# Performance work log

Measured on AMD Instinct MI355X. Metric: run time of the kernel, lower is better.

## Reference

```python
import jax, jax.numpy as jnp
import numpy as np

N = 131072   # total nodes
G = 4096     # graphs
E = 524288   # directed bond edges
C = 96       # hidden_channels
L = 8        # num_layers
F_IN = 64    # atom features
NT = 5       # targets


def setup_inputs() -> dict:
    key = jax.random.key(0)
    ks = jax.random.split(key, 32)
    def rn(k, shape, s=0.05):
        return jax.random.normal(k, shape, jnp.float32) * s
    inp = {
        'x': jax.random.normal(ks[0], (N, F_IN), jnp.float32),
        'edge_index': jax.random.randint(ks[1], (2, E), 0, N),
        'batch': jnp.sort(jax.random.randint(ks[2], (N,), 0, G)),
        'num_graphs': G,
        # atom encoder
        'enc_w': rn(ks[3], (F_IN, C)), 'enc_b': rn(ks[4], (C,)),
        # virtual node embedding + MLP (Linear->BN->SiLU->Linear)
        'vn_emb': rn(ks[5], (C,)),
        'vn_w1': rn(ks[6], (C, C)), 'vn_b1': rn(ks[7], (C,)),
        'vn_g1': 1.0 + rn(ks[8], (C,)), 'vn_be1': rn(ks[9], (C,)),
        'vn_w2': rn(ks[10], (C, C)), 'vn_b2': rn(ks[11], (C,)),
        # per-layer GIN MLP (Linear C->2C, BN, SiLU, Linear 2C->C) stacked over L
        'conv_w1': rn(ks[12], (L, C, 2 * C)), 'conv_b1': rn(ks[13], (L, 2 * C)),
        'conv_g1': 1.0 + rn(ks[14], (L, 2 * C)), 'conv_be1': rn(ks[15], (L, 2 * C)),
        'conv_w2': rn(ks[16], (L, 2 * C, C)), 'conv_b2': rn(ks[17], (L, C)),
        # per-layer outer BatchNorm
        'bn_g': 1.0 + rn(ks[18], (L, C)), 'bn_b': rn(ks[19], (L, C)),
        # head: C->C/2 (BN,SiLU) -> C/4 (BN,SiLU) -> NT
        'h_w1': rn(ks[20], (C, C // 2)), 'h_b1': rn(ks[21], (C // 2,)),
        'h_g1': 1.0 + rn(ks[22], (C // 2,)), 'h_be1': rn(ks[23], (C // 2,)),
        'h_w2': rn(ks[24], (C // 2, C // 4)), 'h_b2': rn(ks[25], (C // 4,)),
        'h_g2': 1.0 + rn(ks[26], (C // 4,)), 'h_be2': rn(ks[27], (C // 4,)),
        'h_w3': rn(ks[28], (C // 4, NT)), 'h_b3': rn(ks[29], (NT,)),
    }
    return inp


def _bn(x, g, b, eps=1e-5):
    # training-mode BatchNorm1d: biased batch variance (matches torch normalization)
    m = x.mean(0)
    v = x.var(0)
    return (x - m) * jax.lax.rsqrt(v + eps) * g + b


def reference(x, edge_index, batch, num_graphs, enc_w, enc_b, vn_emb,
              vn_w1, vn_b1, vn_g1, vn_be1, vn_w2, vn_b2,
              conv_w1, conv_b1, conv_g1, conv_be1, conv_w2, conv_b2,
              bn_g, bn_b,
              h_w1, h_b1, h_g1, h_be1, h_w2, h_b2, h_g2, h_be2, h_w3, h_b3):
    n = x.shape[0]
    gN = int(num_graphs)
    c = enc_w.shape[1]
    nl = conv_w1.shape[0]

    h = x @ enc_w + enc_b                                   # [n, C]
    vn = jnp.broadcast_to(vn_emb, (gN, c))                  # virtual node feats
    h = jnp.concatenate([h, vn], 0)                         # [n+gN, C]

    # vectorized virtual-node edges: (n+batch[i]) <-> i, both directions
    node_ids = jnp.arange(n, dtype=batch.dtype)
    vidx = n + batch
    src = jnp.concatenate([edge_index[0], vidx, node_ids])
    tgt = jnp.concatenate([edge_index[1], node_ids, vidx])
    total = n + gN

    for i in range(nl):
        # GINConv, eps=0: MLP(x + sum_neighbors)
        agg = jax.ops.segment_sum(h[src], tgt, num_segments=total)
        z = h + agg
        z = z @ conv_w1[i] + conv_b1[i]
        z = jax.nn.silu(_bn(z, conv_g1[i], conv_be1[i]))
        z = z @ conv_w2[i] + conv_b2[i]
        z = jax.nn.silu(_bn(z, bn_g[i], bn_b[i]))           # outer BN + SiLU (dropout=eval)
        h = z if i == 0 else h + z                          # residual after layer 0
        if i < nl - 1:
            v = h[n:]
            v = jax.nn.silu(_bn(v @ vn_w1 + vn_b1, vn_g1, vn_be1)) @ vn_w2 + vn_b2
            h = jnp.concatenate([h[:n], v], 0)

    hn = h[:n]
    sums = jax.ops.segment_sum(hn, batch, num_segments=gN)
    counts = jax.ops.segment_sum(jnp.ones((n,), hn.dtype), batch, num_segments=gN)
    pooled = sums / jnp.maximum(counts, 1.0)[:, None]       # global_mean_pool

    z = jax.nn.silu(_bn(pooled @ h_w1 + h_b1, h_g1, h_be1))
    z = jax.nn.silu(_bn(z @ h_w2 + h_b2, h_g2, h_be2))
    return z @ h_w3 + h_b3                                  # [G, 5]
```

## Files before the change

### kernel.cpp

```cpp
#include <hip/hip_runtime.h>
#include <hip/hip_bf16.h>

constexpr int N_   = 131072;
constexpr int G_   = 4096;
constexpr int E_   = 524288;
constexpr int C_   = 96;
constexpr int L_   = 8;
constexpr int FIN_ = 64;
constexpr int TOT_ = N_ + G_;

typedef __attribute__((ext_vector_type(8))) short short8v;
typedef __attribute__((ext_vector_type(4))) float f32x4;
using bf16 = __hip_bfloat16;

__device__ __forceinline__ float silu_f(float y) { return y / (1.f + __expf(-y)); }
__device__ __forceinline__ float toF(float x) { return x; }
__device__ __forceinline__ float toF(bf16 x)  { return __bfloat162float(x); }
__device__ __forceinline__ float bfbits2f(short s) {
  return __uint_as_float(((unsigned)(unsigned short)s) << 16);
}
__device__ __forceinline__ short f2bfbits(float f) {
  bf16 b = __float2bfloat16(f);
  return *reinterpret_cast<short*>(&b);
}
__device__ __forceinline__ void atomAddD(double* p, double v) { unsafeAtomicAdd(p, v); }

static inline int gblk(long n) { return (int)((n + 255) / 256); }

__global__ __launch_bounds__(256) void k_prep(const float* __restrict__ enc_w,
    const float* __restrict__ conv_w1, const float* __restrict__ conv_w2,
    const float* __restrict__ vn_w1, const float* __restrict__ vn_w2,
    bf16* __restrict__ encwT, bf16* __restrict__ w1T, bf16* __restrict__ w2T,
    bf16* __restrict__ vnw1T, bf16* __restrict__ vnw2T) {
  int idx = blockIdx.x * 256 + threadIdx.x;
  const float* src; bf16* dst; int Kd, Nd, local;
  if (idx < 6144)        { src = enc_w;   dst = encwT; Kd = 64;  Nd = 96;  local = idx; }
  else if (idx < 153600) { src = conv_w1; dst = w1T;   Kd = 96;  Nd = 192; local = idx - 6144; }
  else if (idx < 301056) { src = conv_w2; dst = w2T;   Kd = 192; Nd = 96;  local = idx - 153600; }
  else if (idx < 310272) { src = vn_w1;   dst = vnw1T; Kd = 96;  Nd = 96;  local = idx - 301056; }
  else if (idx < 319488) { src = vn_w2;   dst = vnw2T; Kd = 96;  Nd = 96;  local = idx - 310272; }
  else return;
  int per = Kd * Nd;
  int i   = local / per;
  int rem = local - i * per;
  int k   = rem / Nd;
  int n   = rem - k * Nd;
  dst[(size_t)i * per + n * Kd + k] = __float2bfloat16(src[local]);
}

__global__ __launch_bounds__(256) void k_deg_count(const int* __restrict__ tgt, int* __restrict__ deg) {
  int e = blockIdx.x * 256 + threadIdx.x;
  if (e >= E_) return;
  atomicAdd(&deg[tgt[e]], 1);
}

__global__ __launch_bounds__(256) void k_scan_local(const int* __restrict__ deg, int* __restrict__ lp,
                                                    int* __restrict__ bsum) {
  __shared__ int s[256];
  int t = threadIdx.x;
  int i = blockIdx.x * 256 + t;
  int v = deg[i];
  s[t] = v;
  __syncthreads();
  for (int off = 1; off < 256; off <<= 1) {
    int x = (t >= off) ? s[t - off] : 0;
    __syncthreads();
    s[t] += x;
    __syncthreads();
  }
  lp[i] = s[t] - v;
  if (t == 255) bsum[blockIdx.x] = s[255];
}

__global__ __launch_bounds__(512) void k_scan_bsum(const int* __restrict__ bsum, int* __restrict__ boff) {
  __shared__ int s[512];
  int t = threadIdx.x;
  int v = bsum[t];
  s[t] = v;
  __syncthreads();
  for (int off = 1; off < 512; off <<= 1) {
    int x = (t >= off) ? s[t - off] : 0;
    __syncthreads();
    s[t] += x;
    __syncthreads();
  }
  boff[t] = s[t] - v;
}

__global__ __launch_bounds__(256) void k_scan_add(int* __restrict__ rs, const int* __restrict__ boff) {
  int i = blockIdx.x * 256 + threadIdx.x;
  if (i > N_) return;
  if (i == N_) { rs[N_] = E_; return; }
  rs[i] += boff[i >> 8];
}

__global__ __launch_bounds__(256) void k_csr_fill(const int* __restrict__ src, const int* __restrict__ tgt,
                                                  const int* __restrict__ rs, int* __restrict__ cur,
                                                  int* __restrict__ ssrc) {
  int e = blockIdx.x * 256 + threadIdx.x;
  if (e >= E_) return;
  int t = tgt[e];
  int pos = atomicAdd(&cur[t], 1);
  ssrc[rs[t] + pos] = src[e];
}

__global__ __launch_bounds__(256) void k_gbounds(const int* __restrict__ batch, int* __restrict__ gstart) {
  int i = blockIdx.x * 256 + threadIdx.x;
  if (i > N_) return;
  if (i == N_) {
    int last = batch[N_ - 1];
    for (int g = last + 1; g <= G_; ++g) gstart[g] = N_;
    return;
  }
  int b  = batch[i];
  int bp = (i == 0) ? -1 : batch[i - 1];
  for (int g = bp + 1; g <= b; ++g) gstart[g] = i;
}

__global__ __launch_bounds__(256) void k_deghist(const int* __restrict__ deg, int* __restrict__ hist) {
  __shared__ int lh[33];
  if (threadIdx.x < 33) lh[threadIdx.x] = 0;
  __syncthreads();
  int i = blockIdx.x * 256 + threadIdx.x;
  if (i < N_) {
    int b = deg[i]; if (b > 32) b = 32;
    atomicAdd(&lh[b], 1);
  }
  __syncthreads();
  if (threadIdx.x < 33 && lh[threadIdx.x] != 0) atomicAdd(&hist[threadIdx.x], lh[threadIdx.x]);
}

__global__ __launch_bounds__(64) void k_degbase(const int* __restrict__ hist, int* __restrict__ base) {
  if (threadIdx.x == 0) {
    int acc = 0;
    for (int b = 0; b < 33; ++b) { base[b] = acc; acc += hist[b]; }
  }
}

__global__ __launch_bounds__(256) void k_permfill(const int* __restrict__ deg, const int* __restrict__ base,
                                                  int* __restrict__ curs, int* __restrict__ perm) {
  __shared__ int lh[33];
  __shared__ int lbase[33];
  if (threadIdx.x < 33) lh[threadIdx.x] = 0;
  __syncthreads();
  int i = blockIdx.x * 256 + threadIdx.x;
  int b = 0, lpos = 0;
  bool act = (i < N_);
  if (act) {
    b = deg[i]; if (b > 32) b = 32;
    lpos = atomicAdd(&lh[b], 1);
  }
  __syncthreads();
  if (threadIdx.x < 33) {
    int cnt = lh[threadIdx.x];
    lbase[threadIdx.x] = cnt ? atomicAdd(&curs[threadIdx.x], cnt) : 0;
  }
  __syncthreads();
  if (act) perm[base[b] + lbase[b] + lpos] = i;
}

__global__ __launch_bounds__(192) void k_vnagg(const bf16* __restrict__ hb, const int* __restrict__ gstart,
                                               bf16* __restrict__ vna) {
  int slot = threadIdx.x / 24;
  int c4   = (threadIdx.x % 24) * 4;
  int g = blockIdx.x * 8 + slot;
  int i0 = gstart[g], i1 = gstart[g + 1];
  float s0 = 0.f, s1 = 0.f, s2 = 0.f, s3 = 0.f;
  for (int i = i0; i < i1; ++i) {
    short4 v = *(const short4*)((const short*)hb + (size_t)i * C_ + c4);
    s0 += bfbits2f(v.x); s1 += bfbits2f(v.y); s2 += bfbits2f(v.z); s3 += bfbits2f(v.w);
  }
  short4 o;
  o.x = f2bfbits(s0); o.y = f2bfbits(s1); o.z = f2bfbits(s2); o.w = f2bfbits(s3);
  *(short4*)((short*)vna + (size_t)g * C_ + c4) = o;
}

template <int K, int NOUT, bool INACT, bool OSTATS, bool AF32, typename OutT>
__global__ __launch_bounds__(512) void k_gemm(const void* __restrict__ Aptr, const bf16* __restrict__ Wt,
                                              const float* __restrict__ bias,
                                              const double* __restrict__ stin,
                                              const float* __restrict__ gam, const float* __restrict__ bet,
                                              float Rin,
                                              OutT* __restrict__ out, double* __restrict__ stout) {
  constexpr int KK  = K / 32;
  constexpr int NT  = NOUT / 16;
  constexpr int UPR = K / 8;
  constexpr int LPR = UPR + 1;
  constexpr int LWB  = NOUT * LPR * 16;
  constexpr int ISCB = INACT ? 2 * K * 4 : 0;
  constexpr int SMB  = LWB + (ISCB > 0 ? ISCB : 1);
  __shared__ __align__(16) char smem[SMB];
  uint4* lw   = reinterpret_cast<uint4*>(smem);
  float* lsc  = reinterpret_cast<float*>(smem + LWB);
  float* lsh  = lsc + K;
  float* ssum = reinterpret_cast<float*>(smem);
  float* sqs  = ssum + 8 * NOUT;

  const uint4* wv = (const uint4*)Wt;
  for (int u = threadIdx.x; u < NOUT * UPR; u += 512) {
    int row = u / UPR, colu = u - row * UPR;
    lw[row * LPR + colu] = wv[u];
  }
  if (INACT) {
    for (int k = threadIdx.x; k < K; k += 512) {
      double mean = stin[k] / (double)Rin;
      double var  = stin[K + k] / (double)Rin - mean * mean;
      float sc = gam[k] * rsqrtf((float)var + 1e-5f);
      lsc[k] = sc;
      lsh[k] = bet[k] - (float)mean * sc;
    }
  }

  int wave = threadIdx.x >> 6, lane = threadIdx.x & 63;
  int m0 = (blockIdx.x * 8 + wave) * 16;
  int lr = lane & 15, lg = lane >> 4;

  short8v a[KK];
  if constexpr (AF32) {
    const float* Arow = (const float*)Aptr + (size_t)(m0 + lr) * K + lg * 8;
#pragma unroll
    for (int kk = 0; kk < KK; ++kk) {
      float4 f0 = *(const float4*)(Arow + kk * 32);
      float4 f1 = *(const float4*)(Arow + kk * 32 + 4);
      a[kk][0] = f2bfbits(f0.x); a[kk][1] = f2bfbits(f0.y);
      a[kk][2] = f2bfbits(f0.z); a[kk][3] = f2bfbits(f0.w);
      a[kk][4] = f2bfbits(f1.x); a[kk][5] = f2bfbits(f1.y);
      a[kk][6] = f2bfbits(f1.z); a[kk][7] = f2bfbits(f1.w);
    }
  } else {
    const short* Arow = (const short*)Aptr + (size_t)(m0 + lr) * K + lg * 8;
#pragma unroll
    for (int kk = 0; kk < KK; ++kk) a[kk] = *(const short8v*)(Arow + kk * 32);
  }

  __syncthreads();

  if (INACT) {
#pragma unroll
    for (int kk = 0; kk < KK; ++kk) {
      int kbase = kk * 32 + lg * 8;
#pragma unroll
      for (int j = 0; j < 8; ++j) {
        float f = bfbits2f(a[kk][j]);
        f = silu_f(fmaf(f, lsc[kbase + j], lsh[kbase + j]));
        a[kk][j] = f2bfbits(f);
      }
    }
  }

  f32x4 acc[NT];
#pragma unroll
  for (int nt = 0; nt < NT; ++nt) acc[nt] = (f32x4){0.f, 0.f, 0.f, 0.f};

#pragma unroll
  for (int nt = 0; nt < NT; ++nt) {
    const short* brow = (const short*)&lw[(nt * 16 + lr) * LPR] + lg * 8;
#pragma unroll
    for (int kk = 0; kk < KK; ++kk) {
      short8v b = *(const short8v*)(brow + kk * 32);
      acc[nt] = __builtin_amdgcn_mfma_f32_16x16x32_bf16(a[kk], b, acc[nt], 0, 0, 0);
    }
  }

  if (OSTATS) __syncthreads();

  int orow = m0 + (lg << 2);
#pragma unroll
  for (int nt = 0; nt < NT; ++nt) {
    int col = nt * 16 + lr;
    float bi = bias[col];
    float s = 0.f, q = 0.f;
#pragma unroll
    for (int r = 0; r < 4; ++r) {
      float y = acc[nt][r] + bi;
      float yb;
      size_t off = (size_t)(orow + r) * NOUT + col;
      if constexpr (sizeof(OutT) == 2) {
        short bits = f2bfbits(y);
        ((short*)out)[off] = bits;
        yb = bfbits2f(bits);
      } else {
        ((float*)out)[off] = y;
        yb = y;
      }
      if (OSTATS) { s += yb; q += yb * yb; }
    }
    if (OSTATS) {
      s += __shfl_xor(s, 16, 64); s += __shfl_xor(s, 32, 64);
      q += __shfl_xor(q, 16, 64); q += __shfl_xor(q, 32, 64);
      if (lg == 0) { ssum[wave * NOUT + col] = s; sqs[wave * NOUT + col] = q; }
    }
  }
  if (OSTATS) {
    __syncthreads();
    int tid = threadIdx.x;
    if (tid < NOUT) {
      float s = 0.f, q = 0.f;
#pragma unroll
      for (int w = 0; w < 8; ++w) { s += ssum[w * NOUT + tid]; q += sqs[w * NOUT + tid]; }
      atomAddD(&stout[tid], (double)s);
      atomAddD(&stout[NOUT + tid], (double)q);
    }
  }
}

template <int K, int NOUT>
__global__ __launch_bounds__(512) void k_gemm_agg(const bf16* __restrict__ hb,
    const int* __restrict__ batch, const int* __restrict__ rs, const int* __restrict__ ssrc,
    const bf16* __restrict__ vna, const int* __restrict__ perm,
    const bf16* __restrict__ Wt, const float* __restrict__ bias,
    bf16* __restrict__ out, double* __restrict__ st) {
  constexpr int KK  = K / 32;
  constexpr int NT  = NOUT / 16;
  constexpr int UPR = K / 8;
  constexpr int LPR = UPR + 1;
  constexpr int LWB = NOUT * LPR * 16;
  __shared__ __align__(16) char smem[LWB];
  uint4* lw   = reinterpret_cast<uint4*>(smem);
  float* ssum = reinterpret_cast<float*>(smem);
  float* sqs  = ssum + 8 * NOUT;

  const uint4* wv = (const uint4*)Wt;
  for (int u = threadIdx.x; u < NOUT * UPR; u += 512) {
    int row = u / UPR, colu = u - row * UPR;
    lw[row * LPR + colu] = wv[u];
  }

  int wave = threadIdx.x >> 6, lane = threadIdx.x & 63;
  int m0 = (blockIdx.x * 8 + wave) * 16;
  int lr = lane & 15, lg = lane >> 4;
  int row = m0 + lr;
  int rowo = (m0 < N_) ? perm[row] : row;
  int koff = lg * 8;

  float av[KK * 8];
#pragma unroll
  for (int t = 0; t < KK * 8; ++t) av[t] = 0.f;

  auto addPtr = [&](const short* p) {
#pragma unroll
    for (int kk = 0; kk < KK; ++kk) {
      short8v v = *(const short8v*)(p + koff + kk * 32);
#pragma unroll
      for (int j = 0; j < 8; ++j) av[kk * 8 + j] += bfbits2f(v[j]);
    }
  };
  auto addPtr2 = [&](const short* p0, const short* p1) {
    short8v v0[KK], v1[KK];
#pragma unroll
    for (int kk = 0; kk < KK; ++kk) {
      v0[kk] = *(const short8v*)(p0 + koff + kk * 32);
      v1[kk] = *(const short8v*)(p1 + koff + kk * 32);
    }
#pragma unroll
    for (int kk = 0; kk < KK; ++kk)
#pragma unroll
      for (int j = 0; j < 8; ++j)
        av[kk * 8 + j] += bfbits2f(v0[kk][j]) + bfbits2f(v1[kk][j]);
  };
  auto hrow = [&](int r) { return (const short*)hb + (size_t)r * K; };

  if (m0 < N_) {
    addPtr2(hrow(rowo), hrow(N_ + batch[rowo]));
    int e = rs[rowo], e1 = rs[rowo + 1];
    for (; e + 2 <= e1; e += 2) addPtr2(hrow(ssrc[e]), hrow(ssrc[e + 1]));
    if (e < e1) addPtr(hrow(ssrc[e]));
  } else {
    addPtr2(hrow(rowo), (const short*)vna + (size_t)(rowo - N_) * K);
  }

  short8v a[KK];
#pragma unroll
  for (int kk = 0; kk < KK; ++kk)
#pragma unroll
    for (int j = 0; j < 8; ++j) a[kk][j] = f2bfbits(av[kk * 8 + j]);

  __syncthreads();

  f32x4 acc[NT];
#pragma unroll
  for (int nt = 0; nt < NT; ++nt) acc[nt] = (f32x4){0.f, 0.f, 0.f, 0.f};

#pragma unroll
  for (int nt = 0; nt < NT; ++nt) {
    const short* brow = (const short*)&lw[(nt * 16 + lr) * LPR] + lg * 8;
#pragma unroll
    for (int kk = 0; kk < KK; ++kk) {
      short8v b = *(const short8v*)(brow + kk * 32);
      acc[nt] = __builtin_amdgcn_mfma_f32_16x16x32_bf16(a[kk], b, acc[nt], 0, 0, 0);
    }
  }

  __syncthreads();

  int rid[4];
#pragma unroll
  for (int r = 0; r < 4; ++r) rid[r] = __shfl(rowo, (lg << 2) + r, 64);

#pragma unroll
  for (int nt = 0; nt < NT; ++nt) {
    int col = nt * 16 + lr;
    float bi = bias[col];
    float s = 0.f, q = 0.f;
#pragma unroll
    for (int r = 0; r < 4; ++r) {
      float y = acc[nt][r] + bi;
      short bits = f2bfbits(y);
      ((short*)out)[(size_t)rid[r] * NOUT + col] = bits;
      float yb = bfbits2f(bits);
      s += yb; q += yb * yb;
    }
    s += __shfl_xor(s, 16, 64); s += __shfl_xor(s, 32, 64);
    q += __shfl_xor(q, 16, 64); q += __shfl_xor(q, 32, 64);
    if (lg == 0) { ssum[wave * NOUT + col] = s; sqs[wave * NOUT + col] = q; }
  }
  __syncthreads();
  int tid = threadIdx.x;
  if (tid < NOUT) {
    float s = 0.f, q = 0.f;
#pragma unroll
    for (int w = 0; w < 8; ++w) { s += ssum[w * NOUT + tid]; q += sqs[w * NOUT + tid]; }
    atomAddD(&st[tid], (double)s);
    atomAddD(&st[NOUT + tid], (double)q);
  }
}

__global__ __launch_bounds__(256) void k_fill_vn(bf16* __restrict__ hb, const float* __restrict__ vn) {
  int idx = blockIdx.x * 256 + threadIdx.x;
  if (idx >= G_ * C_) return;
  int c = idx % C_;
  hb[(size_t)N_ * C_ + idx] = __float2bfloat16(vn[c]);
}

template <int CC, typename T>
__global__ __launch_bounds__(256) void k_bnstats(const T* __restrict__ X, int R, double* __restrict__ st) {
  int c = threadIdx.x;
  float s = 0.f, q = 0.f;
  for (int r = blockIdx.x; r < R; r += gridDim.x) {
    float v = toF(X[(size_t)r * CC + c]);
    s += v;
    q += v * v;
  }
  atomAddD(&st[c], (double)s);
  atomAddD(&st[CC + c], (double)q);
}

template <int CC>
__global__ __launch_bounds__(256) void k_bnfin(const double* __restrict__ st, int R,
    const float* __restrict__ g, const float* __restrict__ be,
    float* __restrict__ scale, float* __restrict__ shift) {
  int c = threadIdx.x;
  if (c >= CC) return;
  double mean = st[c] / R;
  double var  = st[CC + c] / R - mean * mean;
  float sc = g[c] * rsqrtf((float)var + 1e-5f);
  scale[c] = sc;
  shift[c] = be[c] - (float)mean * sc;
}

__global__ __launch_bounds__(256) void k_update(const bf16* __restrict__ Z, bf16* __restrict__ hb,
    const double* __restrict__ st,
    const float* __restrict__ gam, const float* __restrict__ bet, int addResid) {
  __shared__ float lsc[C_], lsh[C_];
  if (threadIdx.x < C_) {
    int c = threadIdx.x;
    double mean = st[c] / (double)TOT_;
    double var  = st[C_ + c] / (double)TOT_ - mean * mean;
    float sc = gam[c] * rsqrtf((float)var + 1e-5f);
    lsc[c] = sc;
    lsh[c] = bet[c] - (float)mean * sc;
  }
  __syncthreads();
  int idx = blockIdx.x * 256 + threadIdx.x;
  if (idx >= TOT_ * C_ / 8) return;
  int cg = idx % (C_ / 8);
  int c0 = cg * 8;
  short8v zv = ((const short8v*)Z)[idx];
  short8v hv = ((const short8v*)hb)[idx];
  short8v o;
#pragma unroll
  for (int j = 0; j < 8; ++j) {
    float y = silu_f(fmaf(bfbits2f(zv[j]), lsc[c0 + j], lsh[c0 + j]));
    float hn = addResid ? (bfbits2f(hv[j]) + y) : y;
    o[j] = f2bfbits(hn);
  }
  ((short8v*)hb)[idx] = o;
}

template <int K, int M, bool INACT>
__global__ __launch_bounds__(256) void k_mm(const float* __restrict__ A,
    const float* __restrict__ W, const float* __restrict__ bias,
    const float* __restrict__ isc, const float* __restrict__ ish,
    float* __restrict__ out, int R) {
  int idx = blockIdx.x * 256 + threadIdx.x;
  if (idx >= R * M) return;
  int row = idx / M;
  int m   = idx - row * M;
  const float* ar = A + (size_t)row * K;
  float s = bias[m];
#pragma unroll 8
  for (int k = 0; k < K; ++k) {
    float a = ar[k];
    if (INACT) a = silu_f(fmaf(a, isc[k], ish[k]));
    s = fmaf(a, W[k * M + m], s);
  }
  out[idx] = s;
}

__global__ __launch_bounds__(256) void k_pool2(const bf16* __restrict__ hb, const int* __restrict__ gstart,
                                               float* __restrict__ pooled) {
  int idx = blockIdx.x * 256 + threadIdx.x;
  if (idx >= G_ * C_) return;
  int g = idx / C_;
  int c = idx - g * C_;
  int i0 = gstart[g], i1 = gstart[g + 1];
  float s = 0.f;
  for (int i = i0; i < i1; ++i) s += toF(hb[(size_t)i * C_ + c]);
  pooled[idx] = s / fmaxf((float)(i1 - i0), 1.0f);
}

extern "C" void kernel_launch(void* const* d_in, const int* in_sizes, int n_in,
                              void* d_out, int out_size, void* d_ws, size_t ws_size,
                              hipStream_t stream) {
  (void)in_sizes; (void)n_in; (void)out_size; (void)ws_size;
  const float* x       = (const float*)d_in[0];
  const int*   ei      = (const int*)d_in[1];
  const int*   batch   = (const int*)d_in[2];
  const float* enc_w   = (const float*)d_in[4];
  const float* enc_b   = (const float*)d_in[5];
  const float* vn_emb  = (const float*)d_in[6];
  const float* vn_w1   = (const float*)d_in[7];
  const float* vn_b1   = (const float*)d_in[8];
  const float* vn_g1   = (const float*)d_in[9];
  const float* vn_be1  = (const float*)d_in[10];
  const float* vn_w2   = (const float*)d_in[11];
  const float* vn_b2   = (const float*)d_in[12];
  const float* conv_w1 = (const float*)d_in[13];
  const float* conv_b1 = (const float*)d_in[14];
  const float* conv_g1 = (const float*)d_in[15];
  const float* conv_be1= (const float*)d_in[16];
  const float* conv_w2 = (const float*)d_in[17];
  const float* conv_b2 = (const float*)d_in[18];
  const float* bn_g    = (const float*)d_in[19];
  const float* bn_b    = (const float*)d_in[20];
  const float* h_w1    = (const float*)d_in[21];
  const float* h_b1    = (const float*)d_in[22];
  const float* h_g1    = (const float*)d_in[23];
  const float* h_be1   = (const float*)d_in[24];
  const float* h_w2    = (const float*)d_in[25];
  const float* h_b2    = (const float*)d_in[26];
  const float* h_g2    = (const float*)d_in[27];
  const float* h_be2   = (const float*)d_in[28];
  const float* h_w3    = (const float*)d_in[29];
  const float* h_b3    = (const float*)d_in[30];
  float* out = (float*)d_out;

  const int* e_src = ei;
  const int* e_tgt = ei + E_;

  char* p = (char*)d_ws;
  auto alloc = [&](size_t bytes) -> char* {
    char* r = p;
    p += (bytes + 15) & ~size_t(15);
    return r;
  };
  bf16*   hbf    = (bf16*)  alloc((size_t)TOT_ * C_ * 2);
  bf16*   vna    = (bf16*)  alloc((size_t)G_ * C_ * 2);
  bf16*   vtb    = (bf16*)  alloc((size_t)G_ * C_ * 2);
  float*  pooled = (float*) alloc((size_t)G_ * C_ * 4);
  float*  t1     = (float*) alloc((size_t)G_ * 48 * 4);
  float*  t2     = (float*) alloc((size_t)G_ * 24 * 4);
  float*  scale1 = (float*) alloc(256 * 4);
  float*  shift1 = (float*) alloc(256 * 4);
  float*  scale2 = (float*) alloc(256 * 4);
  float*  shift2 = (float*) alloc(256 * 4);
  double* stbuf  = (double*)alloc((size_t)26 * 384 * 8);
  bf16*   z1     = (bf16*)  alloc((size_t)TOT_ * 2 * C_ * 2);
  bf16*   z2     = (bf16*)  alloc((size_t)TOT_ * C_ * 2);
  bf16*   encwT  = (bf16*)  alloc((size_t)C_ * FIN_ * 2);
  bf16*   w1T    = (bf16*)  alloc((size_t)L_ * 2 * C_ * C_ * 2);
  bf16*   w2T    = (bf16*)  alloc((size_t)L_ * C_ * 2 * C_ * 2);
  bf16*   vnw1T  = (bf16*)  alloc((size_t)C_ * C_ * 2);
  bf16*   vnw2T  = (bf16*)  alloc((size_t)C_ * C_ * 2);
  int*    deg    = (int*)   alloc((size_t)N_ * 4);
  int*    cur    = (int*)   alloc((size_t)N_ * 4);
  int*    rs     = (int*)   alloc((size_t)(N_ + 1) * 4);
  int*    bsum   = (int*)   alloc(512 * 4);
  int*    boff   = (int*)   alloc(512 * 4);
  int*    ssrc   = (int*)   alloc((size_t)E_ * 4);
  int*    gstart = (int*)   alloc((size_t)(G_ + 1) * 4);
  int*    perm   = (int*)   alloc((size_t)N_ * 4);
  int*    hist   = (int*)   alloc(33 * 4);
  int*    hbase  = (int*)   alloc(33 * 4);
  int*    hcurs  = (int*)   alloc(33 * 4);

  auto ST = [&](int i) { return stbuf + (size_t)i * 384; };

  k_prep<<<gblk(319488), 256, 0, stream>>>(enc_w, conv_w1, conv_w2, vn_w1, vn_w2,
                                           encwT, w1T, w2T, vnw1T, vnw2T);

  hipMemsetAsync(deg, 0, (size_t)N_ * 4, stream);
  hipMemsetAsync(cur, 0, (size_t)N_ * 4, stream);
  hipMemsetAsync(stbuf, 0, (size_t)26 * 384 * 8, stream);
  hipMemsetAsync(hist, 0, 33 * 4, stream);
  hipMemsetAsync(hcurs, 0, 33 * 4, stream);
  k_deg_count<<<gblk(E_), 256, 0, stream>>>(e_tgt, deg);
  k_scan_local<<<N_ / 256, 256, 0, stream>>>(deg, rs, bsum);
  k_scan_bsum<<<1, 512, 0, stream>>>(bsum, boff);
  k_scan_add<<<gblk(N_ + 1), 256, 0, stream>>>(rs, boff);
  k_csr_fill<<<gblk(E_), 256, 0, stream>>>(e_src, e_tgt, rs, cur, ssrc);
  k_gbounds<<<gblk(N_ + 1), 256, 0, stream>>>(batch, gstart);
  k_deghist<<<gblk(N_), 256, 0, stream>>>(deg, hist);
  k_degbase<<<1, 64, 0, stream>>>(hist, hbase);
  k_permfill<<<gblk(N_), 256, 0, stream>>>(deg, hbase, hcurs, perm);

  k_gemm<FIN_, C_, false, false, true, bf16><<<N_ / 128, 512, 0, stream>>>(
      x, encwT, enc_b, nullptr, nullptr, nullptr, 1.f, hbf, nullptr);
  k_fill_vn<<<gblk((long)G_ * C_), 256, 0, stream>>>(hbf, vn_emb);

  for (int i = 0; i < L_; ++i) {
    const bf16*  wt1 = w1T + (size_t)i * 2 * C_ * C_;
    const bf16*  wt2 = w2T + (size_t)i * C_ * 2 * C_;
    const float* b1  = conv_b1 + (size_t)i * 2 * C_;
    const float* g1  = conv_g1 + (size_t)i * 2 * C_;
    const float* be1 = conv_be1+ (size_t)i * 2 * C_;
    const float* b2  = conv_b2 + (size_t)i * C_;
    const float* bg  = bn_g    + (size_t)i * C_;
    const float* bb  = bn_b    + (size_t)i * C_;

    k_vnagg<<<G_ / 8, 192, 0, stream>>>(hbf, gstart, vna);

    k_gemm_agg<C_, 2 * C_><<<TOT_ / 128, 512, 0, stream>>>(
        hbf, batch, rs, ssrc, vna, perm, wt1, b1, z1, ST(i));

    k_gemm<2 * C_, C_, true, true, false, bf16><<<TOT_ / 128, 512, 0, stream>>>(
        z1, wt2, b2, ST(i), g1, be1, (float)TOT_, z2, ST(8 + i));

    k_update<<<(int)((long)TOT_ * C_ / 8 / 256), 256, 0, stream>>>(z2, hbf, ST(8 + i), bg, bb, i > 0);

    if (i < L_ - 1) {
      k_gemm<C_, C_, false, true, false, bf16><<<G_ / 128, 512, 0, stream>>>(
          hbf + (size_t)N_ * C_, vnw1T, vn_b1, nullptr, nullptr, nullptr, 1.f, vtb, ST(16 + i));
      k_gemm<C_, C_, true, false, false, bf16><<<G_ / 128, 512, 0, stream>>>(
          vtb, vnw2T, vn_b2, ST(16 + i), vn_g1, vn_be1, (float)G_,
          hbf + (size_t)N_ * C_, nullptr);
    }
  }

  k_pool2<<<gblk((long)G_ * C_), 256, 0, stream>>>(hbf, gstart, pooled);

  k_mm<C_, 48, false><<<gblk((long)G_ * 48), 256, 0, stream>>>(
      pooled, h_w1, h_b1, nullptr, nullptr, t1, G_);
  k_bnstats<48, float><<<64, 48, 0, stream>>>(t1, G_, ST(23));
  k_bnfin<48><<<1, 48, 0, stream>>>(ST(23), G_, h_g1, h_be1, scale1, shift1);

  k_mm<48, 24, true><<<gblk((long)G_ * 24), 256, 0, stream>>>(
      t1, h_w2, h_b2, scale1, shift1, t2, G_);
  k_bnstats<24, float><<<64, 24, 0, stream>>>(t2, G_, ST(24));
  k_bnfin<24><<<1, 24, 0, stream>>>(ST(24), G_, h_g2, h_be2, scale2, shift2);

  k_mm<24, 5, true><<<gblk((long)G_ * 5), 256, 0, stream>>>(
      t2, h_w3, h_b3, scale2, shift2, out, G_);
}
```

Measured before the change: 1.255 ms.

## Fuse per-graph node-sum aggregation into update kernel via fp32 atomics

Removes the separate per-layer k_vnagg pass that re-reads all node features, accumulating per-graph sums inside k_update with segmented per-block reductions and float atomics into an fp32 buffer. The virtual-node aggregate is kept in fp32 and read directly in the aggregation GEMM. The degree-bucket permutation order is also reversed so high-degree nodes come first. This adds a memset per layer, atomic traffic, and a smaller 192-thread update block with an extra barrier. Float atomics make the sums order-nondeterministic.

```diff
diff --git a/kernel.cpp b/kernel.cpp
--- a/kernel.cpp
+++ b/kernel.cpp
@@ -24,6 +24,7 @@
   return *reinterpret_cast<short*>(&b);
 }
 __device__ __forceinline__ void atomAddD(double* p, double v) { unsafeAtomicAdd(p, v); }
+__device__ __forceinline__ void atomAddF(float* p, float v)  { unsafeAtomicAdd(p, v); }
 
 static inline int gblk(long n) { return (int)((n + 255) / 256); }
 
@@ -133,7 +134,7 @@
 __global__ __launch_bounds__(64) void k_degbase(const int* __restrict__ hist, int* __restrict__ base) {
   if (threadIdx.x == 0) {
     int acc = 0;
-    for (int b = 0; b < 33; ++b) { base[b] = acc; acc += hist[b]; }
+    for (int b = 32; b >= 0; --b) { base[b] = acc; acc += hist[b]; }
   }
 }
 
@@ -160,7 +161,7 @@
 }
 
 __global__ __launch_bounds__(192) void k_vnagg(const bf16* __restrict__ hb, const int* __restrict__ gstart,
-                                               bf16* __restrict__ vna) {
+                                               float* __restrict__ vna) {
   int slot = threadIdx.x / 24;
   int c4   = (threadIdx.x % 24) * 4;
   int g = blockIdx.x * 8 + slot;
@@ -170,9 +171,8 @@
     short4 v = *(const short4*)((const short*)hb + (size_t)i * C_ + c4);
     s0 += bfbits2f(v.x); s1 += bfbits2f(v.y); s2 += bfbits2f(v.z); s3 += bfbits2f(v.w);
   }
-  short4 o;
-  o.x = f2bfbits(s0); o.y = f2bfbits(s1); o.z = f2bfbits(s2); o.w = f2bfbits(s3);
-  *(short4*)((short*)vna + (size_t)g * C_ + c4) = o;
+  float4 o; o.x = s0; o.y = s1; o.z = s2; o.w = s3;
+  *(float4*)(vna + (size_t)g * C_ + c4) = o;
 }
 
 template <int K, int NOUT, bool INACT, bool OSTATS, bool AF32, typename OutT>
@@ -307,7 +307,7 @@
 template <int K, int NOUT>
 __global__ __launch_bounds__(512) void k_gemm_agg(const bf16* __restrict__ hb,
     const int* __restrict__ batch, const int* __restrict__ rs, const int* __restrict__ ssrc,
-    const bf16* __restrict__ vna, const int* __restrict__ perm,
+    const float* __restrict__ vna, const int* __restrict__ perm,
     const bf16* __restrict__ Wt, const float* __restrict__ bias,
     bf16* __restrict__ out, double* __restrict__ st) {
   constexpr int KK  = K / 32;
@@ -366,7 +366,15 @@
     for (; e + 2 <= e1; e += 2) addPtr2(hrow(ssrc[e]), hrow(ssrc[e + 1]));
     if (e < e1) addPtr(hrow(ssrc[e]));
   } else {
-    addPtr2(hrow(rowo), (const short*)vna + (size_t)(rowo - N_) * K);
+    addPtr(hrow(rowo));
+    const float* vp = vna + (size_t)(rowo - N_) * K + koff;
+#pragma unroll
+    for (int kk = 0; kk < KK; ++kk) {
+      float4 f0 = *(const float4*)(vp + kk * 32);
+      float4 f1 = *(const float4*)(vp + kk * 32 + 4);
+      av[kk * 8 + 0] += f0.x; av[kk * 8 + 1] += f0.y; av[kk * 8 + 2] += f0.z; av[kk * 8 + 3] += f0.w;
+      av[kk * 8 + 4] += f1.x; av[kk * 8 + 5] += f1.y; av[kk * 8 + 6] += f1.z; av[kk * 8 + 7] += f1.w;
+    }
   }
 
   short8v a[KK];
@@ -458,33 +466,58 @@
   shift[c] = be[c] - (float)mean * sc;
 }
 
-__global__ __launch_bounds__(256) void k_update(const bf16* __restrict__ Z, bf16* __restrict__ hb,
+__global__ __launch_bounds__(192) void k_update(const bf16* __restrict__ Z, bf16* __restrict__ hb,
     const double* __restrict__ st,
-    const float* __restrict__ gam, const float* __restrict__ bet, int addResid) {
+    const float* __restrict__ gam, const float* __restrict__ bet, int addResid,
+    float* __restrict__ vna, const int* __restrict__ batch, int accvna) {
   __shared__ float lsc[C_], lsh[C_];
-  if (threadIdx.x < C_) {
-    int c = threadIdx.x;
-    double mean = st[c] / (double)TOT_;
-    double var  = st[C_ + c] / (double)TOT_ - mean * mean;
-    float sc = gam[c] * rsqrtf((float)var + 1e-5f);
-    lsc[c] = sc;
-    lsh[c] = bet[c] - (float)mean * sc;
-  }
-  __syncthreads();
-  int idx = blockIdx.x * 256 + threadIdx.x;
-  if (idx >= TOT_ * C_ / 8) return;
-  int cg = idx % (C_ / 8);
+  __shared__ float lh[16][C_];
+  __shared__ int   lbatch[16];
+  int t = threadIdx.x;
+  if (t < C_) {
+    double mean = st[t] / (double)TOT_;
+    double var  = st[C_ + t] / (double)TOT_ - mean * mean;
+    float sc = gam[t] * rsqrtf((float)var + 1e-5f);
+    lsc[t] = sc;
+    lsh[t] = bet[t] - (float)mean * sc;
+  }
+  int r0 = blockIdx.x * 16;
+  int nodeBlk = (r0 < N_);
+  if (accvna && nodeBlk && t < 16) lbatch[t] = batch[r0 + t];
+  __syncthreads();
+
+  int rl = t / 12;
+  int cg = t - rl * 12;
   int c0 = cg * 8;
-  short8v zv = ((const short8v*)Z)[idx];
-  short8v hv = ((const short8v*)hb)[idx];
+  size_t vidx = (size_t)(r0 + rl) * 12 + cg;
+  short8v zv = ((const short8v*)Z)[vidx];
+  short8v hv = ((const short8v*)hb)[vidx];
   short8v o;
+  float hn[8];
 #pragma unroll
   for (int j = 0; j < 8; ++j) {
     float y = silu_f(fmaf(bfbits2f(zv[j]), lsc[c0 + j], lsh[c0 + j]));
-    float hn = addResid ? (bfbits2f(hv[j]) + y) : y;
-    o[j] = f2bfbits(hn);
-  }
-  ((short8v*)hb)[idx] = o;
+    hn[j] = addResid ? (bfbits2f(hv[j]) + y) : y;
+    o[j] = f2bfbits(hn[j]);
+  }
+  ((short8v*)hb)[vidx] = o;
+
+  if (accvna && nodeBlk) {
+#pragma unroll
+    for (int j = 0; j < 8; ++j) lh[rl][c0 + j] = hn[j];
+    __syncthreads();
+    if (t < C_) {
+      int c = t;
+      float run = 0.f;
+      int g = lbatch[0];
+      for (int r = 0; r < 16; ++r) {
+        int gb = lbatch[r];
+        if (gb != g) { atomAddF(&vna[(size_t)g * C_ + c], run); run = 0.f; g = gb; }
+        run += lh[r][c];
+      }
+      atomAddF(&vna[(size_t)g * C_ + c], run);
+    }
+  }
 }
 
 template <int K, int M, bool INACT>
@@ -565,7 +598,7 @@
     return r;
   };
   bf16*   hbf    = (bf16*)  alloc((size_t)TOT_ * C_ * 2);
-  bf16*   vna    = (bf16*)  alloc((size_t)G_ * C_ * 2);
+  float*  vnaf   = (float*) alloc((size_t)G_ * C_ * 4);
   bf16*   vtb    = (bf16*)  alloc((size_t)G_ * C_ * 2);
   float*  pooled = (float*) alloc((size_t)G_ * C_ * 4);
   float*  t1     = (float*) alloc((size_t)G_ * 48 * 4);
@@ -617,6 +650,7 @@
   k_gemm<FIN_, C_, false, false, true, bf16><<<N_ / 128, 512, 0, stream>>>(
       x, encwT, enc_b, nullptr, nullptr, nullptr, 1.f, hbf, nullptr);
   k_fill_vn<<<gblk((long)G_ * C_), 256, 0, stream>>>(hbf, vn_emb);
+  k_vnagg<<<G_ / 8, 192, 0, stream>>>(hbf, gstart, vnaf);
 
   for (int i = 0; i < L_; ++i) {
     const bf16*  wt1 = w1T + (size_t)i * 2 * C_ * C_;
@@ -627,16 +661,17 @@
     const float* b2  = conv_b2 + (size_t)i * C_;
     const float* bg  = bn_g    + (size_t)i * C_;
     const float* bb  = bn_b    + (size_t)i * C_;
-
-    k_vnagg<<<G_ / 8, 192, 0, stream>>>(hbf, gstart, vna);
+    int accvna = (i < L_ - 1);
 
     k_gemm_agg<C_, 2 * C_><<<TOT_ / 128, 512, 0, stream>>>(
-        hbf, batch, rs, ssrc, vna, perm, wt1, b1, z1, ST(i));
+        hbf, batch, rs, ssrc, vnaf, perm, wt1, b1, z1, ST(i));
 
     k_gemm<2 * C_, C_, true, true, false, bf16><<<TOT_ / 128, 512, 0, stream>>>(
         z1, wt2, b2, ST(i), g1, be1, (float)TOT_, z2, ST(8 + i));
 
-    k_update<<<(int)((long)TOT_ * C_ / 8 / 256), 256, 0, stream>>>(z2, hbf, ST(8 + i), bg, bb, i > 0);
+    if (accvna) hipMemsetAsync(vnaf, 0, (size_t)G_ * C_ * 4, stream);
+    k_update<<<TOT_ / 16, 192, 0, stream>>>(z2, hbf, ST(8 + i), bg, bb, i > 0,
+                                            vnaf, batch, accvna);
 
     if (i < L_ - 1) {
       k_gemm<C_, C_, false, true, false, bf16><<<G_ / 128, 512, 0, stream>>>(
```

Result: faster. 1.162 ms (median of 3 runs) (-7.4%).
